# Kernel tuning notes

Measured on AMD Instinct MI355X. Metric: run time of the kernel, lower is better.

Reference implementation:

```python
import jax, jax.numpy as jnp
import numpy as np

NEG = -1.0e30  # finite stand-in for -inf (exp(NEG-x)==0 exactly in fp32, grad-safe)
PRUNE = 5


def setup_inputs() -> dict:
    key = jax.random.key(0)
    k1, k2, k3, k4 = jax.random.split(key, 4)
    B, T, U, V = 8, 192, 193, 512
    logits = jax.random.normal(k1, (B, T, U, V), dtype=jnp.float32)
    log_probs = jax.nn.log_softmax(logits, axis=-1)  # [B,T,U,V]
    targets = jax.random.randint(k2, (B, U - 1), 1, V, dtype=jnp.int32)
    # lengths must satisfy |t_len-u_len| <= PRUNE for the terminal cell to be in-band
    target_lengths = jax.random.randint(k3, (B,), 150, U, dtype=jnp.int32)
    off = jax.random.randint(k4, (B,), -3, 4, dtype=jnp.int32)
    logit_lengths = jnp.clip(target_lengths + off, 1, T).astype(jnp.int32)
    return {"log_probs": log_probs, "targets": targets,
            "logit_lengths": logit_lengths, "target_lengths": target_lengths}


def _rnnt_loss(log_probs, targets, logit_lengths, target_lengths, prune_range=PRUNE):
    B, T, U, V = log_probs.shape
    Ut = targets.shape[1]  # U - 1
    dt = log_probs.dtype

    blank = log_probs[..., 0]  # [B,T,U] p_blank at (t,u)
    # emit[b,t,j] = log_probs[b,t,j,targets[b,j]]
    emit = jnp.take_along_axis(log_probs[:, :, :Ut, :], targets[:, None, :, None], axis=3)[..., 0]  # [B,T,Ut]
    # emit candidate requires t < T: pad a NEG row at t==T
    emit = jnp.concatenate([emit, jnp.full((B, 1, Ut), NEG, dt)], axis=1)  # [B,T+1,Ut]
    # g[b,t,u] = gain entering cell (t,u) from (t,u-1); g[:,:,0] unused
    g_all = jnp.concatenate([jnp.full((B, T + 1, 1), NEG, dt), emit], axis=2)  # [B,T+1,U]
    # blank_pad[:,t,:] = blank[:,t-1,:] (row t pulls blank from frame t-1); t==0 has no blank move
    blank_pad = jnp.concatenate([jnp.full((B, 1, U), NEG, dt), blank], axis=1)  # [B,T+1,U]

    u_idx = jnp.arange(U)

    def band_mask(t):
        # cells the original actually computes on row t
        return ((u_idx[None, :] >= t - prune_range)
                & (u_idx[None, :] <= t + prune_range)
                & (u_idx[None, :] <= target_lengths[:, None]))

    def combine(x, y):
        # linear recurrence r[u] = logaddexp(r[u-1] + g[u], base[u]) as an associative op
        g1, r1 = x
        g2, r2 = y
        return (g1 + g2, jnp.logaddexp(r1 + g2, r2))

    def row_from_base(base, g, t):
        base = jnp.where(band_mask(t), base, NEG)  # out-of-band cells never feed the row
        _, r = jax.lax.associative_scan(combine, (g, base), axis=1)
        return jnp.where(band_mask(t), r, NEG)

    # row 0: alpha[0,0]=0, within-row emit chain
    init_base = jnp.full((B, U), NEG, dt).at[:, 0].set(0.0)
    row0 = row_from_base(init_base, g_all[:, 0], 0)

    def step(prev, xs):
        blank_row, g_row, t = xs
        row = row_from_base(prev + blank_row, g_row, t)  # blank move from row t-1, then emit chain
        return row, row

    ts = jnp.arange(1, T + 1)
    _, rows = jax.lax.scan(step, row0,
                           (blank_pad[:, 1:].transpose(1, 0, 2),
                            g_all[:, 1:].transpose(1, 0, 2), ts))
    rows = jnp.concatenate([row0[None], rows], axis=0)  # [T+1,B,U]

    final = rows[logit_lengths, jnp.arange(B), target_lengths]  # alpha[t_len, u_len]
    return jnp.mean(-final)  # reduction='mean'


def reference(log_probs, targets, logit_lengths, target_lengths):
    return _rnnt_loss(log_probs, targets, logit_lengths, target_lengths)
```

## Files before the change

kernel.cpp:

```cpp
#include <hip/hip_runtime.h>


#define NEGV -1.0e30f

constexpr int Bc = 8, Tc = 192, Uc = 193, Vc = 512;
constexpr int Utc = Uc - 1;
constexpr int ROWS = Tc + 1;

__device__ __forceinline__ float lae(float a, float b) {
    float m = fmaxf(a, b);
    float d = fminf(a, b) - m;
    return m + __logf(1.0f + __expf(d));
}

__global__ void gather_kernel(const float* __restrict__ lp,
                              const int* __restrict__ targets,
                              float* __restrict__ ws,
                              float* __restrict__ out) {
    int tid = blockIdx.x * blockDim.x + threadIdx.x;
    if (tid == 0) out[0] = 0.0f;
    int total = Bc * ROWS * 32;
    if (tid >= total) return;
    int slot = tid & 31;
    int row  = tid >> 5;
    int b = row / ROWS;
    int t = row % ROWS;
    int d = slot & 15;
    int u = t - 5 + d;
    float v = NEGV;
    if (slot < 16) {
        if (t >= 1 && u >= 0 && u <= Uc - 1 && d <= 10)
            v = lp[(((size_t)b * Tc + (t - 1)) * Uc + u) * Vc];
    } else {
        if (t <= Tc - 1 && u >= 1 && u <= Uc - 1 && d <= 10) {
            int tg = targets[b * Utc + (u - 1)];
            v = lp[(((size_t)b * Tc + t) * Uc + (u - 1)) * Vc + tg];
        }
    }
    ws[(size_t)row * 32 + slot] = v;
}

__global__ void __launch_bounds__(64) alpha_kernel(const float* __restrict__ ws,
                                                   const int* __restrict__ logit_len,
                                                   const int* __restrict__ target_len,
                                                   float* __restrict__ out) {
    int b = blockIdx.x;
    int lane = threadIdx.x;
    int tlen = target_len[b];
    int llen = logit_len[b];
    int final_lane = tlen - llen + 5;

    const float* wsb = ws + (size_t)b * ROWS * 32;
    int ls = lane & 15;

    float alpha = NEGV;
    float res = 0.0f;

    float bl_n = wsb[ls];
    float g_n  = wsb[16 + ls];

    for (int t = 0; t <= Tc; ++t) {
        float bl_c = bl_n, g_c = g_n;
        if (t < Tc) {
            bl_n = wsb[(t + 1) * 32 + ls];
            g_n  = wsb[(t + 1) * 32 + 16 + ls];
        }

        int u = t - 5 + lane;
        bool valid = (u >= 0) && (u <= tlen);

        float base;
        if (t == 0) {
            base = (lane == 5) ? 0.0f : NEGV;
        } else {
            float prevA = __shfl_down(alpha, 1, 64);
            if (lane >= 10) prevA = NEGV;
            base = valid ? (prevA + bl_c) : NEGV;
        }

        float g = g_c, r = base;
        #pragma unroll
        for (int s = 1; s <= 8; s <<= 1) {
            float g2 = __shfl_up(g, s, 64);
            float r2 = __shfl_up(r, s, 64);
            if (lane >= s) {
                r = lae(r2 + g, r);
                g = g2 + g;
            }
        }

        alpha = valid ? r : NEGV;

        if (t == llen && lane == final_lane)
            res = -alpha;
    }

    if (lane == final_lane)
        atomicAdd(out, res * (1.0f / Bc));
}

extern "C" void kernel_launch(void* const* d_in, const int* in_sizes, int n_in,
                              void* d_out, int out_size, void* d_ws, size_t ws_size,
                              hipStream_t stream) {
    const float* lp      = (const float*)d_in[0];
    const int* targets   = (const int*)d_in[1];
    const int* llen      = (const int*)d_in[2];
    const int* tlen      = (const int*)d_in[3];
    float* out = (float*)d_out;
    float* ws  = (float*)d_ws;

    int total = Bc * ROWS * 32;
    int blocks = (total + 255) / 256;
    gather_kernel<<<blocks, 256, 0, stream>>>(lp, targets, ws, out);
    alpha_kernel<<<Bc, 64, 0, stream>>>(ws, llen, tlen, out);
}
```

Baseline: 716.4 us.

## Fuse gather into alpha kernel with LDS staging and DPP log-space scan

Merges the gather and alpha-recurrence kernels into one per-batch block. 512 threads first gather the band's blank and emit log-probs into shared memory, then one wavefront runs the recurrence. The scan now precomputes a prefix sum of the emit gains so each step needs only one log-add-exp scan, done with DPP row shifts instead of shuffles. Rows past the logit length are skipped, and the output is zeroed with a memset. The gather now runs on only 8 blocks, so it may lose memory-level parallelism, and the shift-by-prefix-sum scan can lose precision when the values are large.

```diff
diff --git a/kernel.cpp b/kernel.cpp
--- a/kernel.cpp
+++ b/kernel.cpp
@@ -7,110 +7,102 @@
 constexpr int Utc = Uc - 1;
 constexpr int ROWS = Tc + 1;
 
+template <int CTRL>
+__device__ __forceinline__ float dppf(float old, float x) {
+    return __int_as_float(__builtin_amdgcn_update_dpp(
+        __float_as_int(old), __float_as_int(x), CTRL, 0xF, 0xF, false));
+}
+
 __device__ __forceinline__ float lae(float a, float b) {
     float m = fmaxf(a, b);
     float d = fminf(a, b) - m;
     return m + __logf(1.0f + __expf(d));
 }
 
-__global__ void gather_kernel(const float* __restrict__ lp,
-                              const int* __restrict__ targets,
-                              float* __restrict__ ws,
-                              float* __restrict__ out) {
-    int tid = blockIdx.x * blockDim.x + threadIdx.x;
-    if (tid == 0) out[0] = 0.0f;
-    int total = Bc * ROWS * 32;
-    if (tid >= total) return;
-    int slot = tid & 31;
-    int row  = tid >> 5;
-    int b = row / ROWS;
-    int t = row % ROWS;
-    int d = slot & 15;
-    int u = t - 5 + d;
-    float v = NEGV;
-    if (slot < 16) {
-        if (t >= 1 && u >= 0 && u <= Uc - 1 && d <= 10)
-            v = lp[(((size_t)b * Tc + (t - 1)) * Uc + u) * Vc];
-    } else {
-        if (t <= Tc - 1 && u >= 1 && u <= Uc - 1 && d <= 10) {
-            int tg = targets[b * Utc + (u - 1)];
-            v = lp[(((size_t)b * Tc + t) * Uc + (u - 1)) * Vc + tg];
-        }
-    }
-    ws[(size_t)row * 32 + slot] = v;
+__device__ __forceinline__ float prefix_sum16(float g) {
+    g += dppf<0x111>(0.0f, g);
+    g += dppf<0x112>(0.0f, g);
+    g += dppf<0x114>(0.0f, g);
+    g += dppf<0x118>(0.0f, g);
+    return g;
 }
 
-__global__ void __launch_bounds__(64) alpha_kernel(const float* __restrict__ ws,
-                                                   const int* __restrict__ logit_len,
-                                                   const int* __restrict__ target_len,
-                                                   float* __restrict__ out) {
-    int b = blockIdx.x;
-    int lane = threadIdx.x;
-    int tlen = target_len[b];
-    int llen = logit_len[b];
-    int final_lane = tlen - llen + 5;
+__global__ void __launch_bounds__(512) rnnt_fused_kernel(
+        const float* __restrict__ lp, const int* __restrict__ targets,
+        const int* __restrict__ logit_len, const int* __restrict__ target_len,
+        float* __restrict__ out) {
+    __shared__ float2 rowbuf[ROWS * 16];
 
-    const float* wsb = ws + (size_t)b * ROWS * 32;
-    int ls = lane & 15;
+    const int b = blockIdx.x;
+    const int tlen = target_len[b];
+    const int llen = logit_len[b];
+    const int nrows = llen + 1;
+
+    for (int idx = threadIdx.x; idx < nrows * 16; idx += 512) {
+        int t = idx >> 4, d = idx & 15;
+        int u = t - 5 + d;
+        float bl = NEGV;
+        float g = 0.0f;
+        if (d <= 10 && u >= 0 && u <= Uc - 1 && t >= 1)
+            bl = lp[(((size_t)b * Tc + (t - 1)) * Uc + u) * Vc];
+        if (d <= 10 && u >= 1 && u <= Uc - 1 && t <= Tc - 1)
+            g = lp[(((size_t)b * Tc + t) * Uc + (u - 1)) * Vc + targets[b * Utc + (u - 1)]];
+        rowbuf[idx] = make_float2(bl, g);
+    }
+    __syncthreads();
+    if (threadIdx.x >= 64) return;
+
+    const int lane = threadIdx.x;
+    const int ls = lane & 15;
 
     float alpha = NEGV;
-    float res = 0.0f;
+    float2 cur = rowbuf[ls];
+    float G = prefix_sum16(cur.y);
+    float2 nxt;
 
-    float bl_n = wsb[ls];
-    float g_n  = wsb[16 + ls];
-
-    for (int t = 0; t <= Tc; ++t) {
-        float bl_c = bl_n, g_c = g_n;
-        if (t < Tc) {
-            bl_n = wsb[(t + 1) * 32 + ls];
-            g_n  = wsb[(t + 1) * 32 + 16 + ls];
-        }
-
-        int u = t - 5 + lane;
-        bool valid = (u >= 0) && (u <= tlen);
+    for (int t = 0; t <= llen; ++t) {
+        if (t < llen) nxt = rowbuf[(t + 1) * 16 + ls];
 
         float base;
         if (t == 0) {
             base = (lane == 5) ? 0.0f : NEGV;
         } else {
-            float prevA = __shfl_down(alpha, 1, 64);
-            if (lane >= 10) prevA = NEGV;
-            base = valid ? (prevA + bl_c) : NEGV;
+            float prevA = dppf<0x101>(NEGV, alpha);
+            base = prevA + cur.x;
         }
 
-        float g = g_c, r = base;
-        #pragma unroll
-        for (int s = 1; s <= 8; s <<= 1) {
-            float g2 = __shfl_up(g, s, 64);
-            float r2 = __shfl_up(r, s, 64);
-            if (lane >= s) {
-                r = lae(r2 + g, r);
-                g = g2 + g;
-            }
+        float r;
+        if (t == Tc) {
+            r = base;
+        } else {
+            float s = base - G;
+            s = lae(dppf<0x111>(NEGV, s), s);
+            s = lae(dppf<0x112>(NEGV, s), s);
+            s = lae(dppf<0x114>(NEGV, s), s);
+            s = lae(dppf<0x118>(NEGV, s), s);
+            r = s + G;
         }
 
+        int u = t - 5 + lane;
+        bool valid = (lane <= 10) && (u >= 0) && (u <= tlen);
         alpha = valid ? r : NEGV;
 
-        if (t == llen && lane == final_lane)
-            res = -alpha;
+        if (t < llen) { cur = nxt; G = prefix_sum16(cur.y); }
     }
 
-    if (lane == final_lane)
-        atomicAdd(out, res * (1.0f / Bc));
+    if (lane == tlen - llen + 5)
+        atomicAdd(out, alpha * (-1.0f / (float)Bc));
 }
 
 extern "C" void kernel_launch(void* const* d_in, const int* in_sizes, int n_in,
                               void* d_out, int out_size, void* d_ws, size_t ws_size,
                               hipStream_t stream) {
-    const float* lp      = (const float*)d_in[0];
-    const int* targets   = (const int*)d_in[1];
-    const int* llen      = (const int*)d_in[2];
-    const int* tlen      = (const int*)d_in[3];
+    const float* lp    = (const float*)d_in[0];
+    const int* targets = (const int*)d_in[1];
+    const int* llen    = (const int*)d_in[2];
+    const int* tlen    = (const int*)d_in[3];
     float* out = (float*)d_out;
-    float* ws  = (float*)d_ws;
 
-    int total = Bc * ROWS * 32;
-    int blocks = (total + 255) / 256;
-    gather_kernel<<<blocks, 256, 0, stream>>>(lp, targets, ws, out);
-    alpha_kernel<<<Bc, 64, 0, stream>>>(ws, llen, tlen, out);
+    hipMemsetAsync(out, 0, sizeof(float) * out_size, stream);
+    rnnt_fused_kernel<<<Bc, 512, 0, stream>>>(lp, targets, llen, tlen, out);
 }
```

Result: no change. 708.8 us (-1.1%).
